# Kernel optimization log

Hardware: AMD Instinct MI355X
Metric: run time of the kernel (lower is better)

## Reference

```python
import jax, jax.numpy as jnp
import numpy as np
from jax import lax

B, T, D = 8, 4096, 512

def setup_inputs() -> dict:
    key = jax.random.key(0)
    k0, k1, k2 = jax.random.split(key, 3)
    x = jax.random.normal(k0, (B, T, D), dtype=jnp.float32)
    # transform: Linear(2D, 2D) -> GELU -> Linear(2D, D)
    W1 = jax.random.normal(k1, (2 * D, 2 * D), dtype=jnp.float32) * 0.02
    b1 = jnp.zeros((2 * D,), dtype=jnp.float32)
    W2 = jax.random.normal(k2, (D, 2 * D), dtype=jnp.float32) * 0.02
    b2 = jnp.zeros((D,), dtype=jnp.float32)
    return {"x": x, "W1": W1, "b1": b1, "W2": W2, "b2": b2}

def reference(x, W1, b1, W2, b2):
    # x: [B, T, D]. Sequential gated memory update over T, vectorized over B.
    Bb, Tt, Dd = x.shape

    def step(mem, xt):
        # mem, xt: [B, D]
        edge = jnp.concatenate([xt, mem], axis=-1)          # [B, 2D]
        h = jax.nn.gelu(edge @ W1.T + b1, approximate=False)  # exact GELU (torch default)
        proposed = h @ W2.T + b2                             # [B, D]
        g = jax.nn.sigmoid(proposed)
        mem = mem * (1.0 - g) + proposed * g
        return mem, mem

    xs = jnp.swapaxes(x, 0, 1)                               # [T, B, D]
    mem0 = jnp.zeros((Bb, Dd), dtype=x.dtype)
    _, ys = lax.scan(step, mem0, xs)                         # ys: [T, B, D]
    return jnp.swapaxes(ys, 0, 1)                            # [B, T, D]
```

## Files before the change

### kernel.cpp

```cpp
#include <hip/hip_runtime.h>
#include <cmath>

typedef __attribute__((ext_vector_type(4))) float f32x4;
typedef __attribute__((ext_vector_type(8))) short s16x8;
typedef __attribute__((ext_vector_type(4))) short s16x4;
typedef unsigned long long u64;

#define TSTEPS 4096
#define NCU 32

__device__ __forceinline__ short f2bf(float f) {
  unsigned u = __float_as_uint(f);
  unsigned r = (u + 0x7FFFu + ((u >> 16) & 1u)) >> 16;
  return (short)r;
}
__device__ __forceinline__ float bf2f(short s) {
  return __uint_as_float(((unsigned)(unsigned short)s) << 16);
}

__device__ __forceinline__ void bar_lds() {
  __builtin_amdgcn_sched_barrier(0);
  asm volatile("s_waitcnt lgkmcnt(0)" ::: "memory");
  __builtin_amdgcn_s_barrier();
  __builtin_amdgcn_sched_barrier(0);
}

__global__ void __launch_bounds__(256) pre_gemm(
    const float* __restrict__ x, const float* __restrict__ W1,
    const float* __restrict__ b1, float* __restrict__ pre1)
{
  __shared__ float As[16][136];
  __shared__ float Bs[16][136];
  const int tid = threadIdx.x;
  const int m0 = blockIdx.x * 128, j0 = blockIdx.y * 128;
  const int r = tid >> 1, half = tid & 1;
  const int tx = tid & 15, ty = tid >> 4;

  float acc[8][8];
#pragma unroll
  for (int a = 0; a < 8; a++)
#pragma unroll
    for (int b = 0; b < 8; b++) acc[a][b] = 0.f;

  const int row = m0 + r;
  const float* xrow = x + (((size_t)(row & 7) * 4096) + (size_t)(row >> 3)) * 512;
  const float* wrow = W1 + (size_t)(j0 + r) * 1024;

  for (int k0 = 0; k0 < 512; k0 += 16) {
    f32x4 a0 = *(const f32x4*)(xrow + k0 + half * 8);
    f32x4 a1 = *(const f32x4*)(xrow + k0 + half * 8 + 4);
    f32x4 w0 = *(const f32x4*)(wrow + k0 + half * 8);
    f32x4 w1 = *(const f32x4*)(wrow + k0 + half * 8 + 4);
    __syncthreads();
#pragma unroll
    for (int q = 0; q < 4; q++) {
      As[half * 8 + q][r] = a0[q];
      As[half * 8 + 4 + q][r] = a1[q];
      Bs[half * 8 + q][r] = w0[q];
      Bs[half * 8 + 4 + q][r] = w1[q];
    }
    __syncthreads();
#pragma unroll
    for (int kk = 0; kk < 16; kk++) {
      f32x4 ra0 = *(const f32x4*)&As[kk][ty * 8];
      f32x4 ra1 = *(const f32x4*)&As[kk][ty * 8 + 4];
      f32x4 rb0 = *(const f32x4*)&Bs[kk][tx * 8];
      f32x4 rb1 = *(const f32x4*)&Bs[kk][tx * 8 + 4];
#pragma unroll
      for (int a = 0; a < 4; a++)
#pragma unroll
        for (int b = 0; b < 4; b++) {
          acc[a][b]         += ra0[a] * rb0[b];
          acc[a][b + 4]     += ra0[a] * rb1[b];
          acc[a + 4][b]     += ra1[a] * rb0[b];
          acc[a + 4][b + 4] += ra1[a] * rb1[b];
        }
    }
  }
  float bias[8];
#pragma unroll
  for (int b = 0; b < 8; b++) bias[b] = b1[j0 + tx * 8 + b];

  const int tt = (m0 >> 3) + ty;
  const int col0 = j0 + tx * 8;
  const int c2 = col0 >> 5, jl0 = col0 & 31;
  float* dst = pre1 + (size_t)tt * 8192 + (size_t)c2 * 256 + jl0;
#pragma unroll
  for (int a = 0; a < 8; a++) {
    f32x4 v0, v1;
#pragma unroll
    for (int b = 0; b < 4; b++) { v0[b] = acc[a][b] + bias[b]; v1[b] = acc[a][b + 4] + bias[b + 4]; }
    *(f32x4*)(dst + a * 32) = v0;
    *(f32x4*)(dst + a * 32 + 4) = v1;
  }
}

__global__ void __launch_bounds__(256) seq_scan(
    const float* __restrict__ W1, const float* __restrict__ W2,
    const float* __restrict__ b2, const float* __restrict__ pre1,
    float* __restrict__ out, float* __restrict__ accbuf,
    unsigned* __restrict__ bar)
{
  const int c = blockIdx.x;
  const int tid = threadIdx.x;
  const int l = tid & 63;
  const int w = tid >> 6;

  extern __shared__ char lds[];
  short* w1bh = (short*)lds;
  short* w1bl = w1bh + 32 * 520;
  short* w2h  = w1bl + 32 * 520;
  short* w2l  = w2h + 512 * 36;
  short* memh = w2l + 512 * 36;
  short* meml = memh + 9 * 520;
  short* hh   = meml + 9 * 520;
  short* hl   = hh + 9 * 40;
  float* scr  = (float*)(hl + 9 * 40);

  for (int e = tid; e < 32 * 128; e += 256) {
    int jl = e >> 7, k4 = (e & 127) << 2;
    f32x4 v = *(const f32x4*)(W1 + (size_t)(c * 32 + jl) * 1024 + 512 + k4);
#pragma unroll
    for (int q = 0; q < 4; q++) {
      short hi = f2bf(v[q]);
      w1bh[jl * 520 + k4 + q] = hi;
      w1bl[jl * 520 + k4 + q] = f2bf(v[q] - bf2f(hi));
    }
  }
  for (int e = tid; e < 512 * 8; e += 256) {
    int i = e >> 3, j4 = (e & 7) << 2;
    f32x4 v = *(const f32x4*)(W2 + (size_t)i * 1024 + c * 32 + j4);
#pragma unroll
    for (int q = 0; q < 4; q++) {
      short hi = f2bf(v[q]);
      w2h[i * 36 + j4 + q] = hi;
      w2l[i * 36 + j4 + q] = f2bf(v[q] - bf2f(hi));
    }
  }
  for (int e = tid; e < 9 * 520; e += 256) { memh[e] = 0; meml[e] = 0; }
  for (int e = tid; e < 9 * 40; e += 256)  { hh[e] = 0; hl[e] = 0; }

  const int mg = tid >> 5;
  const int i0own = (tid & 31) * 16;
  float memr[16];
  float b2r[16];
#pragma unroll
  for (int q = 0; q < 16; q++) { memr[q] = 0.f; b2r[q] = b2[i0own + q]; }

  const int jt = w & 1, kh = w >> 1;
  const int m_ep = (l >> 4) * 4;
  const bool ep = (w < 2) && (l < 32);
  const float* p1base = pre1 + (size_t)c * 256 + m_ep * 32 + jt * 16 + (l & 15);
  float p1r[4];
  if (ep) {
#pragma unroll
    for (int rr = 0; rr < 4; rr++) p1r[rr] = p1base[rr * 32];
  }

  const int arow = ((l & 15) < 8) ? (l & 15) : 8;
  const int aoff = arow * 520 + (l >> 4) * 8;
  const int boff = (jt * 16 + (l & 15)) * 520 + (l >> 4) * 8;
  const int haoff = arow * 40 + (l >> 4) * 8;

  __syncthreads();

  for (int t = 0; t < TSTEPS; t++) {
    {
      f32x4 a0 = {0.f,0.f,0.f,0.f}, a1 = a0, a2 = a0;
#pragma unroll
      for (int ks = 0; ks < 8; ks++) {
        const int ko = kh * 256 + ks * 32;
        s16x8 ah = *(const s16x8*)(memh + aoff + ko);
        s16x8 al = *(const s16x8*)(meml + aoff + ko);
        s16x8 bh = *(const s16x8*)(w1bh + boff + ko);
        s16x8 bl = *(const s16x8*)(w1bl + boff + ko);
        a0 = __builtin_amdgcn_mfma_f32_16x16x32_bf16(ah, bh, a0, 0, 0, 0);
        a1 = __builtin_amdgcn_mfma_f32_16x16x32_bf16(al, bh, a1, 0, 0, 0);
        a2 = __builtin_amdgcn_mfma_f32_16x16x32_bf16(ah, bl, a2, 0, 0, 0);
      }
      f32x4 acc = a0 + a1 + a2;
      if (w >= 2) *(f32x4*)(scr + (w - 2) * 256 + l * 4) = acc;
      bar_lds();
      if (w < 2) {
        acc += *(const f32x4*)(scr + w * 256 + l * 4);
        if (l < 32) {
#pragma unroll
          for (int rr = 0; rr < 4; rr++) {
            float xv = acc[rr] + p1r[rr];
            float hv = 0.5f * xv * (1.0f + erff(xv * 0.70710678118654752f));
            short hhi = f2bf(hv);
            hh[(m_ep + rr) * 40 + jt * 16 + (l & 15)] = hhi;
            hl[(m_ep + rr) * 40 + jt * 16 + (l & 15)] = f2bf(hv - bf2f(hhi));
          }
        }
      }
    }
    bar_lds();

    {
      float* accw = accbuf + (size_t)(t & 3) * 4096;
      s16x8 ha = *(const s16x8*)(hh + haoff);
      s16x8 hb = *(const s16x8*)(hl + haoff);
      const int n0 = w * 128;
#pragma unroll
      for (int tt = 0; tt < 8; tt++) {
        const int tl = (tt + c) & 7;
        const int icol = n0 + tl * 16 + (l & 15);
        const int woff = icol * 36 + (l >> 4) * 8;
        s16x8 bh, bl;
        *(s16x4*)&bh = *(const s16x4*)(w2h + woff);
        *((s16x4*)&bh + 1) = *(const s16x4*)(w2h + woff + 4);
        *(s16x4*)&bl = *(const s16x4*)(w2l + woff);
        *((s16x4*)&bl + 1) = *(const s16x4*)(w2l + woff + 4);
        f32x4 p0 = {0.f,0.f,0.f,0.f}, p1 = p0, p2 = p0;
        p0 = __builtin_amdgcn_mfma_f32_16x16x32_bf16(ha, bh, p0, 0, 0, 0);
        p1 = __builtin_amdgcn_mfma_f32_16x16x32_bf16(hb, bh, p1, 0, 0, 0);
        p2 = __builtin_amdgcn_mfma_f32_16x16x32_bf16(ha, bl, p2, 0, 0, 0);
        f32x4 p = p0 + p1 + p2;
        if (l < 32) {
          const int mrow = (l >> 4) * 4;
#pragma unroll
          for (int rr = 0; rr < 4; rr++)
            atomicAdd(accw + ((mrow + rr) << 9) + icol, p[rr]);
        }
      }
    }

    __syncthreads();
    if (tid == 0)
      __hip_atomic_fetch_add(bar, 1u, __ATOMIC_RELAXED, __HIP_MEMORY_SCOPE_AGENT);

    if (tid < 64) {
      u64* z = (u64*)accbuf + (size_t)((t + 2) & 3) * 2048 + c * 64 + tid;
      __hip_atomic_store(z, 0ull, __ATOMIC_RELAXED, __HIP_MEMORY_SCOPE_AGENT);
    }

    if (ep && t + 1 < TSTEPS) {
      const float* pb = p1base + (size_t)(t + 1) * 8192;
#pragma unroll
      for (int rr = 0; rr < 4; rr++) p1r[rr] = pb[rr * 32];
    }

    if (tid == 0) {
      const unsigned target = (unsigned)(NCU * (t + 1));
      while (__hip_atomic_load(bar, __ATOMIC_RELAXED, __HIP_MEMORY_SCOPE_AGENT) < target) {}
    }
    __syncthreads();

    {
      const u64* av = (const u64*)accbuf + (size_t)(t & 3) * 2048;
      u64 vals[8];
#pragma unroll
      for (int q8 = 0; q8 < 8; q8++)
        vals[q8] = __hip_atomic_load(av + tid * 8 + q8, __ATOMIC_RELAXED, __HIP_MEMORY_SCOPE_AGENT);
      float nmv[16];
#pragma unroll
      for (int q8 = 0; q8 < 8; q8++) {
#pragma unroll
        for (int hlf = 0; hlf < 2; hlf++) {
          const int q = 2 * q8 + hlf;
          float v = __uint_as_float((unsigned)(hlf ? (vals[q8] >> 32) : vals[q8]));
          float prop = v + b2r[q];
          float g = 1.0f / (1.0f + __expf(-prop));
          float nm = memr[q] + g * (prop - memr[q]);
          memr[q] = nm;
          nmv[q] = nm;
        }
      }
      s16x8 vh0, vl0, vh1, vl1;
#pragma unroll
      for (int q = 0; q < 8; q++) {
        short hi = f2bf(nmv[q]);
        vh0[q] = hi; vl0[q] = f2bf(nmv[q] - bf2f(hi));
        short hi2 = f2bf(nmv[q + 8]);
        vh1[q] = hi2; vl1[q] = f2bf(nmv[q + 8] - bf2f(hi2));
      }
      *(s16x8*)(memh + mg * 520 + i0own) = vh0;
      *(s16x8*)(memh + mg * 520 + i0own + 8) = vh1;
      *(s16x8*)(meml + mg * 520 + i0own) = vl0;
      *(s16x8*)(meml + mg * 520 + i0own + 8) = vl1;
      if ((tid & 31) == c) {
        float* op = out + ((size_t)mg * TSTEPS + t) * 512 + i0own;
#pragma unroll
        for (int q4 = 0; q4 < 4; q4++) {
          f32x4 v;
#pragma unroll
          for (int j = 0; j < 4; j++) v[j] = nmv[q4 * 4 + j];
          *(f32x4*)(op + q4 * 4) = v;
        }
      }
    }
    bar_lds();
  }
}

extern "C" void kernel_launch(void* const* d_in, const int* in_sizes, int n_in,
                              void* d_out, int out_size, void* d_ws, size_t ws_size,
                              hipStream_t stream) {
  const float* x  = (const float*)d_in[0];
  const float* W1 = (const float*)d_in[1];
  const float* b1 = (const float*)d_in[2];
  const float* W2 = (const float*)d_in[3];
  const float* b2 = (const float*)d_in[4];
  float* out = (float*)d_out;
  char* ws = (char*)d_ws;

  float*    accbuf = (float*)(ws + 0);
  unsigned* bar    = (unsigned*)(ws + 65536);
  float*    pre1   = (float*)(ws + (1u << 20));

  hipMemsetAsync(ws, 0, 65536 + 256, stream);

  dim3 gp(256, 8);
  pre_gemm<<<gp, dim3(256), 0, stream>>>(x, W1, b1, pre1);

  const int LDS_BYTES = 162496;
  hipFuncSetAttribute((const void*)seq_scan,
                      hipFuncAttributeMaxDynamicSharedMemorySize, LDS_BYTES);
  seq_scan<<<dim3(NCU), dim3(256), LDS_BYTES, stream>>>(
      W1, W2, b2, pre1, out, accbuf, bar);
}
```

Baseline: 19.28 ms.

## Shard cross-block atomic accumulators and drop the intra-step K-split barrier

```diff
diff --git a/kernel.cpp b/kernel.cpp
--- a/kernel.cpp
+++ b/kernel.cpp
@@ -115,7 +115,6 @@
   short* meml = memh + 9 * 520;
   short* hh   = meml + 9 * 520;
   short* hl   = hh + 9 * 40;
-  float* scr  = (float*)(hl + 9 * 40);
 
   for (int e = tid; e < 32 * 128; e += 256) {
     int jl = e >> 7, k4 = (e & 127) << 2;
@@ -147,10 +146,9 @@
 #pragma unroll
   for (int q = 0; q < 16; q++) { memr[q] = 0.f; b2r[q] = b2[i0own + q]; }
 
-  const int jt = w & 1, kh = w >> 1;
   const int m_ep = (l >> 4) * 4;
   const bool ep = (w < 2) && (l < 32);
-  const float* p1base = pre1 + (size_t)c * 256 + m_ep * 32 + jt * 16 + (l & 15);
+  const float* p1base = pre1 + (size_t)c * 256 + m_ep * 32 + (w & 1) * 16 + (l & 15);
   float p1r[4];
   if (ep) {
 #pragma unroll
@@ -159,17 +157,18 @@
 
   const int arow = ((l & 15) < 8) ? (l & 15) : 8;
   const int aoff = arow * 520 + (l >> 4) * 8;
-  const int boff = (jt * 16 + (l & 15)) * 520 + (l >> 4) * 8;
+  const int boff = ((w & 1) * 16 + (l & 15)) * 520 + (l >> 4) * 8;
   const int haoff = arow * 40 + (l >> 4) * 8;
+  const int shard = c & 3;
 
   __syncthreads();
 
   for (int t = 0; t < TSTEPS; t++) {
-    {
+    if (w < 2) {
       f32x4 a0 = {0.f,0.f,0.f,0.f}, a1 = a0, a2 = a0;
 #pragma unroll
-      for (int ks = 0; ks < 8; ks++) {
-        const int ko = kh * 256 + ks * 32;
+      for (int ks = 0; ks < 16; ks++) {
+        const int ko = ks * 32;
         s16x8 ah = *(const s16x8*)(memh + aoff + ko);
         s16x8 al = *(const s16x8*)(meml + aoff + ko);
         s16x8 bh = *(const s16x8*)(w1bh + boff + ko);
@@ -179,26 +178,25 @@
         a2 = __builtin_amdgcn_mfma_f32_16x16x32_bf16(ah, bl, a2, 0, 0, 0);
       }
       f32x4 acc = a0 + a1 + a2;
-      if (w >= 2) *(f32x4*)(scr + (w - 2) * 256 + l * 4) = acc;
-      bar_lds();
-      if (w < 2) {
-        acc += *(const f32x4*)(scr + w * 256 + l * 4);
-        if (l < 32) {
-#pragma unroll
-          for (int rr = 0; rr < 4; rr++) {
-            float xv = acc[rr] + p1r[rr];
-            float hv = 0.5f * xv * (1.0f + erff(xv * 0.70710678118654752f));
-            short hhi = f2bf(hv);
-            hh[(m_ep + rr) * 40 + jt * 16 + (l & 15)] = hhi;
-            hl[(m_ep + rr) * 40 + jt * 16 + (l & 15)] = f2bf(hv - bf2f(hhi));
-          }
-        }
-      }
+      if (l < 32) {
+#pragma unroll
+        for (int rr = 0; rr < 4; rr++) {
+          float xv = acc[rr] + p1r[rr];
+          float hv = 0.5f * xv * (1.0f + erff(xv * 0.70710678118654752f));
+          short hhi = f2bf(hv);
+          hh[(m_ep + rr) * 40 + (w & 1) * 16 + (l & 15)] = hhi;
+          hl[(m_ep + rr) * 40 + (w & 1) * 16 + (l & 15)] = f2bf(hv - bf2f(hhi));
+        }
+      }
+    } else {
+      u64* z = (u64*)accbuf + (size_t)((t + 2) & 3) * 8192 + c * 256 + (tid - 128) * 2;
+      __hip_atomic_store(z,     0ull, __ATOMIC_RELAXED, __HIP_MEMORY_SCOPE_AGENT);
+      __hip_atomic_store(z + 1, 0ull, __ATOMIC_RELAXED, __HIP_MEMORY_SCOPE_AGENT);
     }
     bar_lds();
 
     {
-      float* accw = accbuf + (size_t)(t & 3) * 4096;
+      float* accw = accbuf + ((size_t)(t & 3) * 4 + shard) * 4096;
       s16x8 ha = *(const s16x8*)(hh + haoff);
       s16x8 hb = *(const s16x8*)(hl + haoff);
       const int n0 = w * 128;
@@ -230,11 +228,6 @@
     if (tid == 0)
       __hip_atomic_fetch_add(bar, 1u, __ATOMIC_RELAXED, __HIP_MEMORY_SCOPE_AGENT);
 
-    if (tid < 64) {
-      u64* z = (u64*)accbuf + (size_t)((t + 2) & 3) * 2048 + c * 64 + tid;
-      __hip_atomic_store(z, 0ull, __ATOMIC_RELAXED, __HIP_MEMORY_SCOPE_AGENT);
-    }
-
     if (ep && t + 1 < TSTEPS) {
       const float* pb = p1base + (size_t)(t + 1) * 8192;
 #pragma unroll
@@ -248,18 +241,26 @@
     __syncthreads();
 
     {
-      const u64* av = (const u64*)accbuf + (size_t)(t & 3) * 2048;
-      u64 vals[8];
-#pragma unroll
-      for (int q8 = 0; q8 < 8; q8++)
-        vals[q8] = __hip_atomic_load(av + tid * 8 + q8, __ATOMIC_RELAXED, __HIP_MEMORY_SCOPE_AGENT);
+      const u64* av = (const u64*)accbuf + (size_t)(t & 3) * 8192;
+      u64 vals[4][8];
+#pragma unroll
+      for (int s = 0; s < 4; s++)
+#pragma unroll
+        for (int q8 = 0; q8 < 8; q8++)
+          vals[s][q8] = __hip_atomic_load(av + s * 2048 + tid * 8 + q8,
+                                          __ATOMIC_RELAXED, __HIP_MEMORY_SCOPE_AGENT);
       float nmv[16];
 #pragma unroll
       for (int q8 = 0; q8 < 8; q8++) {
 #pragma unroll
         for (int hlf = 0; hlf < 2; hlf++) {
           const int q = 2 * q8 + hlf;
-          float v = __uint_as_float((unsigned)(hlf ? (vals[q8] >> 32) : vals[q8]));
+          float v = 0.f;
+#pragma unroll
+          for (int s = 0; s < 4; s++) {
+            u64 x8 = vals[s][q8];
+            v += __uint_as_float((unsigned)(hlf ? (x8 >> 32) : x8));
+          }
           float prop = v + b2r[q];
           float g = 1.0f / (1.0f + __expf(-prop));
           float nm = memr[q] + g * (prop - memr[q]);
@@ -306,15 +307,15 @@
   char* ws = (char*)d_ws;
 
   float*    accbuf = (float*)(ws + 0);
-  unsigned* bar    = (unsigned*)(ws + 65536);
-  float*    pre1   = (float*)(ws + (1u << 20));
-
-  hipMemsetAsync(ws, 0, 65536 + 256, stream);
+  unsigned* bar    = (unsigned*)(ws + 262144);
+  float*    pre1   = (float*)(ws + (1u << 21));
+
+  hipMemsetAsync(ws, 0, 262144 + 256, stream);
 
   dim3 gp(256, 8);
   pre_gemm<<<gp, dim3(256), 0, stream>>>(x, W1, b1, pre1);
 
-  const int LDS_BYTES = 162496;
+  const int LDS_BYTES = 160448;
   hipFuncSetAttribute((const void*)seq_scan,
                       hipFuncAttributeMaxDynamicSharedMemorySize, LDS_BYTES);
   seq_scan<<<dim3(NCU), dim3(256), LDS_BYTES, stream>>>(
```

Result: slower. 28.62 ms (+48.4%).
